# Optimization experiments

Measured on AMD Instinct MI355X. Metric: run time of the kernel, lower is better.

## Reference

```python
import jax, jax.numpy as jnp
import numpy as np

SMOOTH = 1e-6
ALPHA = 0.25
GAMMA = 2.0
W_DICE, W_CLDICE, W_FOCAL = 0.1, 0.7, 0.2


def _shift(x, dy, dx):
    # x: [B,H,W]; value of neighbor at (i+dy, j+dx), zero-padded borders
    H, W = x.shape[1], x.shape[2]
    p = jnp.pad(x, ((0, 0), (1, 1), (1, 1)))
    return p[:, 1 + dy:1 + dy + H, 1 + dx:1 + dx + W]


def _thin_subiter(img, sub):
    # One Zhang-Suen thinning sub-iteration (matches skimage 2D skeletonize algorithm).
    p2 = _shift(img, -1, 0)   # N
    p3 = _shift(img, -1, 1)   # NE
    p4 = _shift(img, 0, 1)    # E
    p5 = _shift(img, 1, 1)    # SE
    p6 = _shift(img, 1, 0)    # S
    p7 = _shift(img, 1, -1)   # SW
    p8 = _shift(img, 0, -1)   # W
    p9 = _shift(img, -1, -1)  # NW
    nbrs = [p2, p3, p4, p5, p6, p7, p8, p9]
    B = sum(nbrs)
    # A = number of 0->1 transitions in circular sequence p2..p9
    A = sum(((nbrs[k] < 0.5) & (nbrs[(k + 1) % 8] > 0.5)).astype(jnp.int32)
            for k in range(8))
    c1 = (B >= 2.0) & (B <= 6.0)
    c2 = (A == 1)
    if sub == 0:
        c3 = (p2 * p4 * p6) == 0.0
        c4 = (p4 * p6 * p8) == 0.0
    else:
        c3 = (p2 * p4 * p8) == 0.0
        c4 = (p2 * p6 * p8) == 0.0
    remove = (img > 0.5) & c1 & c2 & c3 & c4
    return jnp.where(remove, 0.0, img)


def _skeletonize(img):
    # img: [B,H,W] float32 in {0,1}. Iterate thinning to convergence.
    def body(state):
        cur, _ = state
        new = _thin_subiter(_thin_subiter(cur, 0), 1)
        return (new, jnp.any(new != cur))

    out, _ = jax.lax.while_loop(lambda s: s[1], body, (img, jnp.array(True)))
    return out


def setup_inputs() -> dict:
    key = jax.random.key(0)
    k1, k2 = jax.random.split(key)
    logits = jax.random.normal(k1, (16, 2, 512, 512), dtype=jnp.float32)
    true = jax.random.randint(k2, (16, 512, 512), 0, 2, dtype=jnp.int32)
    return {"logits": logits, "true": true}


def reference(logits, true):
    probs = jax.nn.softmax(logits, axis=1)

    # --- clDice (detached in torch original -> stop_gradient, non-differentiable) ---
    pred = jax.lax.stop_gradient(probs[:, 1])          # [B,H,W]
    pred_bin = (pred > 0.5).astype(jnp.float32)
    true_bin = (true > 0).astype(jnp.float32)
    pred_skel = _skeletonize(pred_bin)
    true_skel = _skeletonize(true_bin)
    inter = jnp.sum(pred_skel * true_skel, axis=(1, 2))
    denom = jnp.sum(pred_skel, axis=(1, 2)) + jnp.sum(true_skel, axis=(1, 2))
    cldice = (2.0 * inter + SMOOTH) / (denom + SMOOTH)
    cldice_loss = 1.0 - jnp.mean(cldice)

    # --- Dice ---
    n_cls = probs.shape[1]
    t1h = jax.nn.one_hot(true, n_cls, axis=1, dtype=probs.dtype)  # [B,C,H,W]
    inter_d = jnp.sum(probs * t1h, axis=(0, 2, 3))
    card = jnp.sum(probs + t1h, axis=(0, 2, 3))
    dice_loss = 1.0 - jnp.mean((2.0 * inter_d + SMOOTH) / (card + SMOOTH))

    # --- Focal ---
    logp = jax.nn.log_softmax(logits, axis=1)
    ce = -jnp.take_along_axis(logp, true[:, None, :, :].astype(jnp.int32), axis=1)[:, 0]
    pt = jnp.exp(-ce)
    focal_loss = jnp.mean(ALPHA * (1.0 - pt) ** GAMMA * ce)

    return W_CLDICE * cldice_loss + W_DICE * dice_loss + W_FOCAL * focal_loss
```

## Files before the change

### kernel.cpp

```cpp
#include <hip/hip_runtime.h>
#include <hip/hip_bf16.h>

typedef unsigned long long u64;

#define NB 16
#define HW 512
#define PIX_PER_B (HW * HW)
#define NPIX (NB * PIX_PER_B)
#define WORDS_PER_B (PIX_PER_B / 64)
#define SROW 9

#define WS_PART_OFF 1024
#define WS_MASK_OFF 32768
#define WS_NEED_MASKS (WS_MASK_OFF + (size_t)2 * NB * WORDS_PER_B * 8)

#define RED_BLOCKS 224
#define FB_BLOCKS 512


__device__ __forceinline__ void fa3(u64 a, u64 b, u64 c, u64& s, u64& cy) {
  u64 x = a ^ b;
  s = x ^ c;
  cy = (a & b) | (c & x);
}

__device__ __forceinline__ u64 thin_word(u64 nm, u64 nl, u64 nr,
                                         u64 cm, u64 cl, u64 cr,
                                         u64 sm, u64 sl, u64 sr, int sub) {
  u64 p2 = nm;
  u64 p3 = (nm >> 1) | (nr << 63);
  u64 p4 = (cm >> 1) | (cr << 63);
  u64 p5 = (sm >> 1) | (sr << 63);
  u64 p6 = sm;
  u64 p7 = (sm << 1) | (sl >> 63);
  u64 p8 = (cm << 1) | (cl >> 63);
  u64 p9 = (nm << 1) | (nl >> 63);

  u64 u1, v1, u2, v2, ss, sc, cs, cc;
  fa3(p2, p3, p4, u1, v1);
  fa3(p5, p6, p7, u2, v2);
  u64 u3 = p8 ^ p9, v3 = p8 & p9;
  fa3(u1, u2, u3, ss, sc);
  fa3(v1, v2, v3, cs, cc);
  u64 w  = sc & cs;
  u64 b1 = sc ^ cs;
  u64 b2 = cc ^ w;
  u64 b3 = cc & w;
  u64 cond1 = (sc | cs | cc) & ~(b3 | (b2 & b1 & ss));

  u64 t0 = ~p2 & p3, t1 = ~p3 & p4, t2 = ~p4 & p5, t3 = ~p5 & p6;
  u64 t4 = ~p6 & p7, t5 = ~p7 & p8, t6 = ~p8 & p9, t7 = ~p9 & p2;
  u64 as1, ac1, as2, ac2, Ass, Asc, Acs, Acc;
  fa3(t0, t1, t2, as1, ac1);
  fa3(t3, t4, t5, as2, ac2);
  u64 as3 = t6 ^ t7, ac3 = t6 & t7;
  fa3(as1, as2, as3, Ass, Asc);
  fa3(ac1, ac2, ac3, Acs, Acc);
  u64 cond2 = Ass & ~(Asc | Acs | Acc);

  u64 cond3, cond4;
  if (sub == 0) { cond3 = ~(p2 & p4 & p6); cond4 = ~(p4 & p6 & p8); }
  else          { cond3 = ~(p2 & p4 & p8); cond4 = ~(p2 & p6 & p8); }

  u64 rem = cm & cond1 & cond2 & cond3 & cond4;
  return cm & ~rem;
}


__global__ __launch_bounds__(256) void mask_kernel(
    const float* __restrict__ logits, const int* __restrict__ tr,
    unsigned char* __restrict__ ws) {
  int tid = threadIdx.x, blk = blockIdx.x;
  u64* predM = (u64*)(ws + WS_MASK_OFF);
  u64* trueM = predM + (size_t)NB * WORDS_PER_B;
  if (blk == 0 && tid < 56) ((u64*)(ws + 64))[tid] = 0;
#pragma unroll 4
  for (int it = 0; it < 64; ++it) {
    int g = (it * 256 + blk) * 256 + tid;
    int b = g >> 18;
    int r = g & (PIX_PER_B - 1);
    const float* lp = logits + (size_t)b * 2 * PIX_PER_B + r;
    float l0 = lp[0], l1 = lp[PIX_PER_B];
    int t = tr[g];
    u64 pm = __ballot(l1 > l0);
    u64 tm = __ballot(t > 0);
    if ((tid & 63) == 0) { predM[g >> 6] = pm; trueM[g >> 6] = tm; }
  }
}


__global__ __launch_bounds__(1024) void fused_kernel(
    const float* __restrict__ logits, const int* __restrict__ tr,
    unsigned char* __restrict__ ws) {
  __shared__ u64 S[HW * SROW];
  __shared__ unsigned char dirty[2][130];
  __shared__ int flag;
  __shared__ double red[16][6];

  int tid  = threadIdx.x;
  int lane = tid & 63;

  if (blockIdx.x < 32) {
    int b    = blockIdx.x;
    int img  = b & 15;
    int wcol = tid & 7;
    int s    = tid >> 3;
    int r0   = s * 4;

    u64* region = (u64*)(ws + WS_MASK_OFF) + (size_t)b * WORDS_PER_B;
    u64* clSp = (u64*)(ws + 192);
    u64* clSt = (u64*)(ws + 320);

#pragma unroll
    for (int i = 0; i < 4; i++)
      S[(r0 + i) * SROW + wcol] = region[(r0 + i) * 8 + wcol];
    if (tid < 130) {
      unsigned char init = (tid >= 1 && tid <= 128) ? 1 : 0;
      dirty[0][tid] = init;
      dirty[1][tid] = init;
    }
    if (tid == 0) flag = 0;
    __syncthreads();

    auto loadRow = [&](int r, u64& m, u64& l, u64& rr) {
      if (r < 0 || r >= HW) { m = 0; l = 0; rr = 0; return; }
      const u64* row = &S[r * SROW];
      m  = row[wcol];
      l  = wcol ? row[wcol - 1] : 0ULL;
      rr = (wcol < 7) ? row[wcol + 1] : 0ULL;
    };

    auto subIter = [&](int sub, int db, int pairTag) {
      unsigned char* dOut = dirty[db ^ 1];
      bool laneActive = (dirty[0][s] | dirty[0][s + 1] | dirty[0][s + 2] |
                         dirty[1][s] | dirty[1][s + 1] | dirty[1][s + 2]) != 0;
      u64 wmask = __ballot(laneActive);
      bool stripCh = false;
      u64 nw[4];
      bool doit = (wmask != 0);
      if (doit) {
        u64 am, al, ar, bm, bl, br, cmv, clv, crv, oldc[4];
        loadRow(r0 - 1, am, al, ar);
        loadRow(r0,     bm, bl, br);
#pragma unroll
        for (int i = 0; i < 4; i++) {
          loadRow(r0 + 1 + i, cmv, clv, crv);
          oldc[i] = bm;
          nw[i] = thin_word(am, al, ar, bm, bl, br, cmv, clv, crv, sub);
          am = bm; al = bl; ar = br;
          bm = cmv; bl = clv; br = crv;
        }
        bool ch = false;
#pragma unroll
        for (int i = 0; i < 4; i++) ch |= (nw[i] != oldc[i]);
        u64 bal = __ballot(ch);
        stripCh = ((bal >> (lane & 56)) & 0xFFULL) != 0;
      }
      __syncthreads();
      if (doit) {
#pragma unroll
        for (int i = 0; i < 4; i++) S[(r0 + i) * SROW + wcol] = nw[i];
      }
      if ((tid & 7) == 0) {
        dOut[s + 1] = stripCh ? 1 : 0;
        if (stripCh) flag = pairTag;
      }
      __syncthreads();
    };

    for (int pair = 1; pair <= 2000; ++pair) {
      subIter(0, 0, pair);
      subIter(1, 1, pair);
      if (flag != pair) break;
    }

    u64 cnt = 0;
#pragma unroll
    for (int i = 0; i < 4; i++) {
      u64 w = S[(r0 + i) * SROW + wcol];
      region[(r0 + i) * 8 + wcol] = w;
      cnt += (u64)__popcll(w);
    }
    for (int o = 32; o; o >>= 1) cnt += __shfl_down(cnt, o, 64);
    if (lane == 0) atomicAdd((b < NB ? clSp : clSt) + img, cnt);

  } else {
    int rb = blockIdx.x - 32;
    double a0 = 0, a1 = 0, s0 = 0, s1 = 0, cnt = 0, fo = 0;
    for (int g = rb * 1024 + tid; g < NPIX; g += RED_BLOCKS * 1024) {
      int b = g >> 18;
      int r = g & (PIX_PER_B - 1);
      const float* lp = logits + (size_t)b * 2 * PIX_PER_B + r;
      float l0 = lp[0], l1 = lp[PIX_PER_B];
      int t = tr[g];
      float m = fmaxf(l0, l1);
      float e0 = expf(l0 - m), e1 = expf(l1 - m);
      float ssum = e0 + e1;
      float p0 = e0 / ssum, p1 = e1 / ssum;
      if (t) a1 += (double)p1; else a0 += (double)p0;
      s0 += (double)p0;
      s1 += (double)p1;
      cnt += (double)t;
      float lse = m + logf(ssum);
      float ce = lse - (t ? l1 : l0);
      float pt = t ? p1 : p0;
      float om = 1.0f - pt;
      fo += (double)(0.25f * om * om * ce);
    }
    double v[6] = {a0, a1, s0, s1, cnt, fo};
    int wv = tid >> 6;
#pragma unroll
    for (int j = 0; j < 6; j++) {
      double x = v[j];
      for (int o = 32; o; o >>= 1) x += __shfl_down(x, o, 64);
      if (lane == 0) red[wv][j] = x;
    }
    __syncthreads();
    if (tid < 6) {
      double t6 = 0;
      for (int w = 0; w < 16; w++) t6 += red[w][tid];
      double* part = (double*)(ws + WS_PART_OFF) + (size_t)rb * 6;
      part[tid] = t6;
    }
  }
}


__global__ __launch_bounds__(256) void inter_kernel(unsigned char* __restrict__ ws) {
  int i = blockIdx.x;
  int tid = threadIdx.x;
  const u64* p = (const u64*)(ws + WS_MASK_OFF) + (size_t)i * WORDS_PER_B;
  const u64* t = p + (size_t)NB * WORDS_PER_B;
  u64 acc = 0;
  for (int w = tid; w < WORDS_PER_B; w += 256) acc += (u64)__popcll(p[w] & t[w]);
  for (int o = 32; o; o >>= 1) acc += __shfl_down(acc, o, 64);
  __shared__ u64 r[4];
  if ((tid & 63) == 0) r[tid >> 6] = acc;
  __syncthreads();
  if (tid == 0) {
    u64* clInter = (u64*)(ws + 64);
    clInter[i] = r[0] + r[1] + r[2] + r[3];
  }
}


__global__ __launch_bounds__(512) void finalize_kernel(unsigned char* __restrict__ ws,
                                                       float* __restrict__ out, int count) {
  int tid = threadIdx.x;
  const double* part = (const double*)(ws + WS_PART_OFF);
  double v[6] = {0, 0, 0, 0, 0, 0};
  if (tid < count) {
#pragma unroll
    for (int j = 0; j < 6; j++) v[j] = part[(size_t)tid * 6 + j];
  }
  __shared__ double red[8][6];
  int lane = tid & 63, wv = tid >> 6;
#pragma unroll
  for (int j = 0; j < 6; j++) {
    double x = v[j];
    for (int o = 32; o; o >>= 1) x += __shfl_down(x, o, 64);
    if (lane == 0) red[wv][j] = x;
  }
  __syncthreads();
  if (tid == 0) {
    double t[6] = {0, 0, 0, 0, 0, 0};
    for (int w = 0; w < 8; w++)
      for (int j = 0; j < 6; j++) t[j] += red[w][j];
    double a0 = t[0], a1 = t[1], s0 = t[2], s1 = t[3], cnt = t[4], fo = t[5];

    const double N = (double)NPIX;
    double cnt0 = N - cnt;
    double card0 = s0 + cnt0, card1 = s1 + cnt;
    double dice = 0.5 * ((2.0 * a0 + 1e-6) / (card0 + 1e-6) +
                         (2.0 * a1 + 1e-6) / (card1 + 1e-6));
    double diceL = 1.0 - dice;
    double focalL = fo / N;

    const u64* clInter = (const u64*)(ws + 64);
    const u64* clSp    = (const u64*)(ws + 192);
    const u64* clSt    = (const u64*)(ws + 320);
    double cs = 0;
    for (int b = 0; b < NB; b++) {
      double inter = (double)clInter[b];
      double den = (double)(clSp[b] + clSt[b]);
      cs += (2.0 * inter + 1e-6) / (den + 1e-6);
    }
    double clL = 1.0 - cs / (double)NB;

    out[0] = (float)(0.7 * clL + 0.1 * diceL + 0.2 * focalL);
  }
}


__global__ __launch_bounds__(256) void loss_reduce_fb_kernel(
    const float* __restrict__ logits, const int* __restrict__ tr,
    unsigned char* __restrict__ ws) {
  int tid = threadIdx.x;
  double a0 = 0, a1 = 0, s0 = 0, s1 = 0, cnt = 0, fo = 0;
  const int iters = NPIX / (FB_BLOCKS * 256);
  for (int it = 0; it < iters; ++it) {
    int g = (it * FB_BLOCKS + (int)blockIdx.x) * 256 + tid;
    int b = g >> 18;
    int r = g & (PIX_PER_B - 1);
    const float* lp = logits + (size_t)b * 2 * PIX_PER_B + r;
    float l0 = lp[0], l1 = lp[PIX_PER_B];
    int t = tr[g];
    float m = fmaxf(l0, l1);
    float e0 = expf(l0 - m), e1 = expf(l1 - m);
    float s = e0 + e1;
    float p0 = e0 / s, p1 = e1 / s;
    if (t) a1 += (double)p1; else a0 += (double)p0;
    s0 += (double)p0;
    s1 += (double)p1;
    cnt += (double)t;
    float lse = m + logf(s);
    float ce = lse - (t ? l1 : l0);
    float pt = t ? p1 : p0;
    float om = 1.0f - pt;
    fo += (double)(0.25f * om * om * ce);
  }
  __shared__ double red[4][6];
  double v[6] = {a0, a1, s0, s1, cnt, fo};
  int lane = tid & 63, wv = tid >> 6;
#pragma unroll
  for (int j = 0; j < 6; j++) {
    double x = v[j];
    for (int o = 32; o; o >>= 1) x += __shfl_down(x, o, 64);
    if (lane == 0) red[wv][j] = x;
  }
  __syncthreads();
  if (tid < 6) {
    double* part = (double*)(ws + WS_PART_OFF) + (size_t)blockIdx.x * 6;
    part[tid] = red[0][tid] + red[1][tid] + red[2][tid] + red[3][tid];
  }
}

__global__ __launch_bounds__(1024) void skel_combined_kernel(
    const float* __restrict__ logits, const int* __restrict__ tr,
    unsigned char* __restrict__ ws) {
  __shared__ u64 S[HW * SROW];
  __shared__ int flag;

  int tid  = threadIdx.x;
  int b    = blockIdx.x;
  int wcol = tid & 7;
  int r0   = (tid >> 3) * 4;
  int lane = tid & 63;

  u64* clInter = (u64*)(ws + 64);
  u64* clSp    = (u64*)(ws + 192);
  u64* clSt    = (u64*)(ws + 320);

  auto buildPred = [&]() {
    const float* lp0 = logits + (size_t)b * 2 * PIX_PER_B;
    const float* lp1 = lp0 + PIX_PER_B;
    for (int k = 0; k < PIX_PER_B / 1024; k++) {
      int p = k * 1024 + tid;
      u64 msk = __ballot(lp1[p] > lp0[p]);
      if (lane == 0) { int wi = p >> 6; S[(wi >> 3) * SROW + (wi & 7)] = msk; }
    }
    __syncthreads();
  };
  auto buildTrue = [&]() {
    const int* tp = tr + (size_t)b * PIX_PER_B;
    for (int k = 0; k < PIX_PER_B / 1024; k++) {
      int p = k * 1024 + tid;
      u64 msk = __ballot(tp[p] > 0);
      if (lane == 0) { int wi = p >> 6; S[(wi >> 3) * SROW + (wi & 7)] = msk; }
    }
    __syncthreads();
  };

  auto loadRow = [&](int r, u64& m, u64& l, u64& rr) {
    if (r < 0 || r >= HW) { m = 0; l = 0; rr = 0; return; }
    const u64* row = &S[r * SROW];
    m  = row[wcol];
    l  = wcol ? row[wcol - 1] : 0ULL;
    rr = (wcol < 7) ? row[wcol + 1] : 0ULL;
  };

  auto subIter = [&](int sub) {
    u64 am, al, ar, bm, bl, br, cmv, clv, crv;
    u64 nw[4], oldc[4];
    loadRow(r0 - 1, am, al, ar);
    loadRow(r0,     bm, bl, br);
#pragma unroll
    for (int i = 0; i < 4; i++) {
      loadRow(r0 + 1 + i, cmv, clv, crv);
      oldc[i] = bm;
      nw[i] = thin_word(am, al, ar, bm, bl, br, cmv, clv, crv, sub);
      am = bm; al = bl; ar = br;
      bm = cmv; bl = clv; br = crv;
    }
    __syncthreads();
    bool ch = false;
#pragma unroll
    for (int i = 0; i < 4; i++) {
      S[(r0 + i) * SROW + wcol] = nw[i];
      ch |= (nw[i] != oldc[i]);
    }
    if (ch) flag = 1;
    __syncthreads();
  };

  auto thinConverge = [&]() {
    for (int it = 0; it < 2000; ++it) {
      if (tid == 0) flag = 0;
      __syncthreads();
      subIter(0);
      subIter(1);
      int f = flag;
      __syncthreads();
      if (!f) break;
    }
  };

  buildPred();
  thinConverge();
  u64 pr[4];
  u64 spL = 0;
#pragma unroll
  for (int i = 0; i < 4; i++) {
    pr[i] = S[(r0 + i) * SROW + wcol];
    spL += (u64)__popcll(pr[i]);
  }
  __syncthreads();

  buildTrue();
  thinConverge();
  u64 stL = 0, inL = 0;
#pragma unroll
  for (int i = 0; i < 4; i++) {
    u64 tw = S[(r0 + i) * SROW + wcol];
    stL += (u64)__popcll(tw);
    inL += (u64)__popcll(tw & pr[i]);
  }

  for (int o = 32; o; o >>= 1) {
    spL += __shfl_down(spL, o, 64);
    stL += __shfl_down(stL, o, 64);
    inL += __shfl_down(inL, o, 64);
  }
  if (lane == 0) {
    atomicAdd(clSp + b, spL);
    atomicAdd(clSt + b, stL);
    atomicAdd(clInter + b, inL);
  }
}


extern "C" void kernel_launch(void* const* d_in, const int* in_sizes, int n_in,
                              void* d_out, int out_size, void* d_ws, size_t ws_size,
                              hipStream_t stream) {
  const float* logits = (const float*)d_in[0];
  const int* tr = (const int*)d_in[1];
  float* out = (float*)d_out;
  unsigned char* ws = (unsigned char*)d_ws;

  if (ws_size >= WS_NEED_MASKS) {
    hipLaunchKernelGGL(mask_kernel, dim3(256), dim3(256), 0, stream, logits, tr, ws);
    hipLaunchKernelGGL(fused_kernel, dim3(32 + RED_BLOCKS), dim3(1024), 0, stream,
                       logits, tr, ws);
    hipLaunchKernelGGL(inter_kernel, dim3(NB), dim3(256), 0, stream, ws);
    hipLaunchKernelGGL(finalize_kernel, dim3(1), dim3(512), 0, stream, ws, out, RED_BLOCKS);
  } else {
    hipMemsetAsync(d_ws, 0, 512, stream);
    hipLaunchKernelGGL(loss_reduce_fb_kernel, dim3(FB_BLOCKS), dim3(256), 0, stream,
                       logits, tr, ws);
    hipLaunchKernelGGL(skel_combined_kernel, dim3(NB), dim3(1024), 0, stream,
                       logits, tr, ws);
    hipLaunchKernelGGL(finalize_kernel, dim3(1), dim3(512), 0, stream, ws, out, FB_BLOCKS);
  }
}
```

Measured before the change: 147.9 us.

## Fuse skeleton intersection into fused kernel via cross-block flag; widen mask kernel grid

Removes the separate inter_kernel launch. Each true-skeleton block waits on a per-image release flag set by the matching pred-skeleton block, then computes the intersection popcount from its own registers against the stored pred skeleton. The mask kernel is also restructured to use 2048 blocks, with each wave loading four words' worth of pixels at once instead of running a 64-iteration loop. The spin-wait relies on the paired blocks being co-resident, and because the done flags are zeroed by mask_kernel, the ordering across launches matters.

```diff
diff --git a/kernel.cpp b/kernel.cpp
--- a/kernel.cpp
+++ b/kernel.cpp
@@ -16,6 +16,8 @@
 
 #define RED_BLOCKS 224
 #define FB_BLOCKS 512
+#define MASK_BLOCKS 2048
+
 
 
 __device__ __forceinline__ void fa3(u64 a, u64 b, u64 c, u64& s, u64& cy) {
@@ -71,20 +73,43 @@
     const float* __restrict__ logits, const int* __restrict__ tr,
     unsigned char* __restrict__ ws) {
   int tid = threadIdx.x, blk = blockIdx.x;
+  int lane = tid & 63;
   u64* predM = (u64*)(ws + WS_MASK_OFF);
   u64* trueM = predM + (size_t)NB * WORDS_PER_B;
-  if (blk == 0 && tid < 56) ((u64*)(ws + 64))[tid] = 0;
-#pragma unroll 4
-  for (int it = 0; it < 64; ++it) {
-    int g = (it * 256 + blk) * 256 + tid;
-    int b = g >> 18;
-    int r = g & (PIX_PER_B - 1);
-    const float* lp = logits + (size_t)b * 2 * PIX_PER_B + r;
-    float l0 = lp[0], l1 = lp[PIX_PER_B];
-    int t = tr[g];
-    u64 pm = __ballot(l1 > l0);
-    u64 tm = __ballot(t > 0);
-    if ((tid & 63) == 0) { predM[g >> 6] = pm; trueM[g >> 6] = tm; }
+  if (blk == 0 && tid < 64) ((u64*)(ws + 64))[tid] = 0;
+
+  int wv = (blk * 256 + tid) >> 6;
+#pragma unroll
+  for (int it = 0; it < 2; ++it) {
+    int T = wv * 2 + it;
+    int P = T << 8;
+    int b = P >> 18;
+    int rbase = (P & (PIX_PER_B - 1)) + lane;
+    const float* lp0 = logits + (size_t)b * 2 * PIX_PER_B;
+    const float* lp1 = lp0 + PIX_PER_B;
+    const int* tp = tr + (size_t)b * PIX_PER_B;
+    float l0v[4], l1v[4];
+    int tv[4];
+#pragma unroll
+    for (int k = 0; k < 4; k++) {
+      int r = rbase + k * 64;
+      l0v[k] = lp0[r];
+      l1v[k] = lp1[r];
+      tv[k] = tp[r];
+    }
+    u64 pw[4], twd[4];
+#pragma unroll
+    for (int k = 0; k < 4; k++) {
+      pw[k] = __ballot(l1v[k] > l0v[k]);
+      twd[k] = __ballot(tv[k] > 0);
+    }
+    if (lane == 0) {
+#pragma unroll
+      for (int k = 0; k < 4; k++) {
+        predM[T * 4 + k] = pw[k];
+        trueM[T * 4 + k] = twd[k];
+      }
+    }
   }
 }
 
@@ -108,8 +133,10 @@
     int r0   = s * 4;
 
     u64* region = (u64*)(ws + WS_MASK_OFF) + (size_t)b * WORDS_PER_B;
-    u64* clSp = (u64*)(ws + 192);
-    u64* clSt = (u64*)(ws + 320);
+    u64* clInter = (u64*)(ws + 64);
+    u64* clSp    = (u64*)(ws + 192);
+    u64* clSt    = (u64*)(ws + 320);
+    u64* done    = (u64*)(ws + 448);
 
 #pragma unroll
     for (int i = 0; i < 4; i++)
@@ -174,15 +201,45 @@
       if (flag != pair) break;
     }
 
+    u64 own[4];
     u64 cnt = 0;
 #pragma unroll
     for (int i = 0; i < 4; i++) {
-      u64 w = S[(r0 + i) * SROW + wcol];
-      region[(r0 + i) * 8 + wcol] = w;
-      cnt += (u64)__popcll(w);
+      own[i] = S[(r0 + i) * SROW + wcol];
+      cnt += (u64)__popcll(own[i]);
     }
     for (int o = 32; o; o >>= 1) cnt += __shfl_down(cnt, o, 64);
-    if (lane == 0) atomicAdd((b < NB ? clSp : clSt) + img, cnt);
+
+    if (b < NB) {
+#pragma unroll
+      for (int i = 0; i < 4; i++) region[(r0 + i) * 8 + wcol] = own[i];
+      if (lane == 0) atomicAdd(clSp + img, cnt);
+      __syncthreads();
+      if (tid == 0) {
+        __threadfence();
+        __hip_atomic_store(&done[img], 1ULL, __ATOMIC_RELEASE, __HIP_MEMORY_SCOPE_AGENT);
+      }
+    } else {
+      if (lane == 0) atomicAdd(clSt + img, cnt);
+      if (tid == 0) {
+        while (__hip_atomic_load(&done[img], __ATOMIC_ACQUIRE,
+                                 __HIP_MEMORY_SCOPE_AGENT) == 0ULL) {
+          __builtin_amdgcn_s_sleep(8);
+        }
+        __threadfence();
+      }
+      __syncthreads();
+      const u64* predRegion = (const u64*)(ws + WS_MASK_OFF) + (size_t)img * WORDS_PER_B;
+      u64 inL = 0;
+#pragma unroll
+      for (int i = 0; i < 4; i++) {
+        u64 pw = __hip_atomic_load(&predRegion[(r0 + i) * 8 + wcol],
+                                   __ATOMIC_RELAXED, __HIP_MEMORY_SCOPE_AGENT);
+        inL += (u64)__popcll(pw & own[i]);
+      }
+      for (int o = 32; o; o >>= 1) inL += __shfl_down(inL, o, 64);
+      if (lane == 0) atomicAdd(clInter + img, inL);
+    }
 
   } else {
     int rb = blockIdx.x - 32;
@@ -222,24 +279,6 @@
       double* part = (double*)(ws + WS_PART_OFF) + (size_t)rb * 6;
       part[tid] = t6;
     }
-  }
-}
-
-
-__global__ __launch_bounds__(256) void inter_kernel(unsigned char* __restrict__ ws) {
-  int i = blockIdx.x;
-  int tid = threadIdx.x;
-  const u64* p = (const u64*)(ws + WS_MASK_OFF) + (size_t)i * WORDS_PER_B;
-  const u64* t = p + (size_t)NB * WORDS_PER_B;
-  u64 acc = 0;
-  for (int w = tid; w < WORDS_PER_B; w += 256) acc += (u64)__popcll(p[w] & t[w]);
-  for (int o = 32; o; o >>= 1) acc += __shfl_down(acc, o, 64);
-  __shared__ u64 r[4];
-  if ((tid & 63) == 0) r[tid >> 6] = acc;
-  __syncthreads();
-  if (tid == 0) {
-    u64* clInter = (u64*)(ws + 64);
-    clInter[i] = r[0] + r[1] + r[2] + r[3];
   }
 }
 
@@ -458,10 +497,10 @@
   unsigned char* ws = (unsigned char*)d_ws;
 
   if (ws_size >= WS_NEED_MASKS) {
-    hipLaunchKernelGGL(mask_kernel, dim3(256), dim3(256), 0, stream, logits, tr, ws);
+    hipLaunchKernelGGL(mask_kernel, dim3(MASK_BLOCKS), dim3(256), 0, stream,
+                       logits, tr, ws);
     hipLaunchKernelGGL(fused_kernel, dim3(32 + RED_BLOCKS), dim3(1024), 0, stream,
                        logits, tr, ws);
-    hipLaunchKernelGGL(inter_kernel, dim3(NB), dim3(256), 0, stream, ws);
     hipLaunchKernelGGL(finalize_kernel, dim3(1), dim3(512), 0, stream, ws, out, RED_BLOCKS);
   } else {
     hipMemsetAsync(d_ws, 0, 512, stream);
```

After: 126.7 us. 14.3% less time.
